# Optimization experiments

Measured on AMD Instinct MI355X. Metric: run time of the kernel, lower is better.

## Reference

```python
import jax, jax.numpy as jnp
import numpy as np

EMB = 1024
NHEAD = 16
HEAD_DIM = EMB // NHEAD  # 64
L = 2048
NEG = -1e30


def setup_inputs() -> dict:
    key = jax.random.key(0)
    ks = jax.random.split(key, 8)
    # xavier_uniform bound for square [EMB, EMB] matrices
    bound = float(np.sqrt(6.0 / (EMB + EMB)))
    def xavier(k):
        return jax.random.uniform(k, (EMB, EMB), jnp.float32, -bound, bound)
    return {
        "q": jax.random.normal(ks[0], (L, EMB), jnp.float32),
        "k": jax.random.normal(ks[1], (L, EMB), jnp.float32),
        "v": jax.random.normal(ks[2], (L, EMB), jnp.float32),
        "mask": jax.random.randint(ks[3], (NHEAD, L, L), 0, 2) > 0,
        "Wq": xavier(ks[4]),
        "Wk": xavier(ks[5]),
        "Wv": xavier(ks[6]),
        "Wo": xavier(ks[7]),
    }


def reference(q, k, v, mask, Wq, Wk, Wv, Wo):
    scaling = HEAD_DIM ** -0.5
    # F.linear(x, W) = x @ W.T ; reshape to [H, L, D]
    Q = (q @ Wq.T).reshape(L, NHEAD, HEAD_DIM).swapaxes(0, 1)
    K = (k @ Wk.T).reshape(L, NHEAD, HEAD_DIM).swapaxes(0, 1)
    V = (v @ Wv.T).reshape(L, NHEAD, HEAD_DIM).swapaxes(0, 1)
    scores = jnp.einsum("hld,hmd->hlm", Q, K) * scaling  # [H, L, L]
    scores = jnp.where(mask, jnp.asarray(NEG, scores.dtype), scores)
    p = jax.nn.softmax(scores, axis=-1)
    # attn_mask=True: multiplicative re-mask after softmax (custom path)
    p = p * (~mask).astype(p.dtype)
    # dropout is a no-op in eval mode
    attn_out = jnp.einsum("hlm,hmd->hld", p, V)  # [H, L, D]
    attn_out = attn_out.swapaxes(0, 1).reshape(L, EMB)
    return attn_out @ Wo.T
```

## Files before the change

kernel.cpp:

```cpp
#include <hip/hip_runtime.h>
#include <stdint.h>

#define EMB   1024
#define NHEAD 16
#define HDIM  64
#define SEQ   2048

typedef unsigned short ushort_t;
typedef unsigned int   uint32;
typedef unsigned long long ull_t;
typedef __attribute__((ext_vector_type(8))) short bfrag;
typedef __attribute__((ext_vector_type(4))) float ffrag;

#define MFMA(a, b, c) __builtin_amdgcn_mfma_f32_16x16x32_bf16((a), (b), (c), 0, 0, 0)

__device__ inline ushort_t f2bf(float f) {
  uint32 u = __float_as_uint(f);
  u += 0x7FFFu + ((u >> 16) & 1u);
  return (ushort_t)(u >> 16);
}
__device__ inline uint32 pack2(float a, float b) {
  return (uint32)f2bf(a) | ((uint32)f2bf(b) << 16);
}

__device__ inline void glds16(const ushort_t* g, ushort_t* l) {
  __builtin_amdgcn_global_load_lds(
      (const __attribute__((address_space(1))) uint32*)(uintptr_t)g,
      (__attribute__((address_space(3))) uint32*)(uintptr_t)l, 16, 0, 0);
}

__global__ void detect_mask_kernel(const uint32* __restrict__ mw, int* __restrict__ flag) {
  uint32 w = mw[threadIdx.x];
  bool is4 = (w == 0u) || (w == 1u) || (w == 0x3F800000u);
  unsigned long long bad = __ballot(!is4);
  if (threadIdx.x == 0) flag[0] = (bad == 0ull) ? 1 : 0;
}

__global__ __launch_bounds__(256) void cvt_all(
    const float4* __restrict__ q,  const float4* __restrict__ k,  const float4* __restrict__ v,
    const float4* __restrict__ wq, const float4* __restrict__ wk, const float4* __restrict__ wv,
    const float4* __restrict__ wo,
    uint2* __restrict__ qb,  uint2* __restrict__ kb,  uint2* __restrict__ vb,
    uint2* __restrict__ wqb, uint2* __restrict__ wkb, uint2* __restrict__ wvb,
    uint2* __restrict__ wob)
{
  int t = blockIdx.x * 256 + threadIdx.x;
  int s = blockIdx.y;
  const float4* src; uint2* dst; int n4;
  switch (s) {
    case 0: src = q;  dst = qb;  n4 = (SEQ * EMB) / 4; break;
    case 1: src = k;  dst = kb;  n4 = (SEQ * EMB) / 4; break;
    case 2: src = v;  dst = vb;  n4 = (SEQ * EMB) / 4; break;
    case 3: src = wq; dst = wqb; n4 = (EMB * EMB) / 4; break;
    case 4: src = wk; dst = wkb; n4 = (EMB * EMB) / 4; break;
    case 5: src = wv; dst = wvb; n4 = (EMB * EMB) / 4; break;
    default: src = wo; dst = wob; n4 = (EMB * EMB) / 4; break;
  }
  if (t >= n4) return;
  float4 f = src[t];
  uint2 o; o.x = pack2(f.x, f.y); o.y = pack2(f.z, f.w);
  dst[t] = o;
}

template<int MODE>
__global__ __launch_bounds__(256) void gemm128(
    const ushort_t* __restrict__ A, const ushort_t* __restrict__ B,
    void* __restrict__ Cp)
{
  __shared__ ushort_t As[128 * 64];
  __shared__ ushort_t Bs[128 * 64];

  const int tid = threadIdx.x, lane = tid & 63, w = tid >> 6;
  const int m0 = blockIdx.y * 128, n0 = blockIdx.x * 128;
  const int wm = (w >> 1) * 64, wn = (w & 1) * 64;
  const int col = lane & 15, g = lane >> 4, kg8 = g * 8;

  int srow[4], scol[4], sdst[4];
  #pragma unroll
  for (int it = 0; it < 4; ++it) {
    int p = w * 256 + it * 64 + lane;
    int row = p >> 3, pc = p & 7;
    srow[it] = row;
    scol[it] = (pc ^ (row & 7)) * 8;
    sdst[it] = p * 8;
  }

  ffrag acc[4][4] = {};

  for (int k0 = 0; k0 < EMB; k0 += 64) {
    __syncthreads();
    #pragma unroll
    for (int it = 0; it < 4; ++it) {
      glds16(A + (size_t)(m0 + srow[it]) * EMB + k0 + scol[it], &As[sdst[it]]);
      glds16(B + (size_t)(n0 + srow[it]) * EMB + k0 + scol[it], &Bs[sdst[it]]);
    }
    __syncthreads();

    #pragma unroll
    for (int c = 0; c < 2; ++c) {
      bfrag av[4], bv[4];
      #pragma unroll
      for (int t = 0; t < 4; ++t) {
        int ra = wm + t * 16 + col;
        av[t] = *(const bfrag*)&As[ra * 64 + ((c * 4 + g) ^ (ra & 7)) * 8];
        int rb = wn + t * 16 + col;
        bv[t] = *(const bfrag*)&Bs[rb * 64 + ((c * 4 + g) ^ (rb & 7)) * 8];
      }
      #pragma unroll
      for (int tm = 0; tm < 4; ++tm)
        #pragma unroll
        for (int tn = 0; tn < 4; ++tn)
          acc[tm][tn] = MFMA(av[tm], bv[tn], acc[tm][tn]);
    }
  }

  const int rbase = g * 4;
  #pragma unroll
  for (int tm = 0; tm < 4; ++tm)
    #pragma unroll
    for (int tn = 0; tn < 4; ++tn)
      #pragma unroll
      for (int r = 0; r < 4; ++r) {
        int m = m0 + wm + tm * 16 + rbase + r;
        int n = n0 + wn + tn * 16 + col;
        float vv = acc[tm][tn][r];
        if (MODE == 0) {
          ((ushort_t*)Cp)[((size_t)(n >> 6) * SEQ + m) * HDIM + (n & 63)] = f2bf(vv);
        } else if (MODE == 1) {
          ((ushort_t*)Cp)[((size_t)(m >> 6) * HDIM + (m & 63)) * SEQ + n] = f2bf(vv);
        } else {
          ((float*)Cp)[(size_t)m * EMB + n] = vv;
        }
      }
}

__global__ __launch_bounds__(256) void attn_mfma(
    const ushort_t* __restrict__ Qb,
    const ushort_t* __restrict__ Kb,
    const ushort_t* __restrict__ Vtb,
    const void* __restrict__ maskp,
    const int* __restrict__ flagp,
    ushort_t* __restrict__ attnb)
{
  __shared__ ushort_t Qs[64][72];
  __shared__ ushort_t Ks[64][72];
  __shared__ ushort_t Vs[64][72];
  __shared__ ushort_t Ps[4][16 * 72];
  __shared__ ushort_t Msk[64][4];

  const int tid  = threadIdx.x;
  const int lane = tid & 63;
  const int w    = tid >> 6;
  const int h    = blockIdx.y;
  const int l0   = blockIdx.x * 64;
  const int use32 = *flagp;
  const int srow = tid >> 2, sseg = (tid & 3) * 16;
  const int col  = lane & 15, g = lane >> 4, kg8 = g * 8, rbase = g * 4;

  const uint32* mask32 = (const uint32*)maskp;
  const unsigned char* mask8 = (const unsigned char*)maskp;

  {
    const uint4* pq = (const uint4*)(Qb + ((size_t)h * SEQ + l0 + srow) * HDIM + sseg);
    uint4 q0 = pq[0], q1 = pq[1];
    *(uint4*)&Qs[srow][sseg] = q0; *(uint4*)&Qs[srow][sseg + 8] = q1;
  }
  __syncthreads();

  bfrag qf[2];
  qf[0] = *(const bfrag*)&Qs[w * 16 + col][kg8];
  qf[1] = *(const bfrag*)&Qs[w * 16 + col][32 + kg8];

  float mrow[4], lrow[4];
  ffrag oacc[4] = {};
  #pragma unroll
  for (int r = 0; r < 4; ++r) { mrow[r] = -1e30f; lrow[r] = 0.f; }

  ushort_t* pq_ = &Ps[w][0];

  for (int kt = 0; kt < SEQ; kt += 64) {
    const uint4* pk = (const uint4*)(Kb + ((size_t)h * SEQ + kt + srow) * HDIM + sseg);
    uint4 k0v = pk[0], k1v = pk[1];
    const uint4* pv = (const uint4*)(Vtb + ((size_t)h * HDIM + srow) * SEQ + kt + sseg);
    uint4 v0v = pv[0], v1v = pv[1];

    ushort_t mv = 0;
    if (use32) {
      const uint4* mp = (const uint4*)(mask32 + ((size_t)h * SEQ + l0 + srow) * SEQ + kt + sseg);
      uint4 a0 = mp[0], a1 = mp[1], a2 = mp[2], a3 = mp[3];
      uint32 aw[16] = {a0.x,a0.y,a0.z,a0.w, a1.x,a1.y,a1.z,a1.w,
                       a2.x,a2.y,a2.z,a2.w, a3.x,a3.y,a3.z,a3.w};
      #pragma unroll
      for (int i = 0; i < 16; ++i) mv |= (ushort_t)((aw[i] != 0u) ? 1u : 0u) << i;
    } else {
      const uint4* bp = (const uint4*)(mask8 + ((size_t)h * SEQ + l0 + srow) * SEQ + kt + sseg);
      uint4 b0 = bp[0];
      uint32 bw[4] = {b0.x, b0.y, b0.z, b0.w};
      #pragma unroll
      for (int i = 0; i < 16; ++i)
        mv |= (ushort_t)((((bw[i >> 2] >> ((i & 3) * 8)) & 0xFFu) != 0u) ? 1u : 0u) << i;
    }

    __syncthreads();
    *(uint4*)&Ks[srow][sseg] = k0v; *(uint4*)&Ks[srow][sseg + 8] = k1v;
    *(uint4*)&Vs[srow][sseg] = v0v; *(uint4*)&Vs[srow][sseg + 8] = v1v;
    Msk[srow][tid & 3] = mv;
    __syncthreads();

    ffrag s[4] = {};
    #pragma unroll
    for (int c = 0; c < 2; ++c)
      #pragma unroll
      for (int tn = 0; tn < 4; ++tn) {
        bfrag kf = *(const bfrag*)&Ks[tn * 16 + col][c * 32 + kg8];
        s[tn] = MFMA(qf[c], kf, s[tn]);
      }

    float sv[4][4];
    float rmax[4] = {-1e30f, -1e30f, -1e30f, -1e30f};
    #pragma unroll
    for (int r = 0; r < 4; ++r) {
      ull_t ms = *(const ull_t*)&Msk[w * 16 + rbase + r][0];
      #pragma unroll
      for (int tn = 0; tn < 4; ++tn) {
        ushort_t m16 = (ushort_t)(ms >> (16 * tn));
        bool msk = ((m16 >> col) & 1) != 0;
        float x = s[tn][r] * 0.125f;
        x = msk ? -1e30f : x;
        sv[tn][r] = x;
        rmax[r] = fmaxf(rmax[r], x);
      }
    }
    #pragma unroll
    for (int r = 0; r < 4; ++r)
      #pragma unroll
      for (int off = 1; off < 16; off <<= 1)
        rmax[r] = fmaxf(rmax[r], __shfl_xor(rmax[r], off, 64));

    float alpha[4], rsum[4] = {0.f, 0.f, 0.f, 0.f};
    #pragma unroll
    for (int r = 0; r < 4; ++r) {
      float mnew = fmaxf(mrow[r], rmax[r]);
      alpha[r] = __expf(mrow[r] - mnew);
      mrow[r] = mnew;
    }

    #pragma unroll
    for (int tn = 0; tn < 4; ++tn)
      #pragma unroll
      for (int r = 0; r < 4; ++r) {
        float p = __expf(sv[tn][r] - mrow[r]);
        rsum[r] += p;
        pq_[(rbase + r) * 72 + tn * 16 + col] = f2bf(p);
      }
    #pragma unroll
    for (int r = 0; r < 4; ++r) {
      #pragma unroll
      for (int off = 1; off < 16; off <<= 1)
        rsum[r] += __shfl_xor(rsum[r], off, 64);
      lrow[r] = lrow[r] * alpha[r] + rsum[r];
    }
    #pragma unroll
    for (int tn = 0; tn < 4; ++tn)
      #pragma unroll
      for (int r = 0; r < 4; ++r)
        oacc[tn][r] *= alpha[r];

    #pragma unroll
    for (int c = 0; c < 2; ++c) {
      bfrag af = *(const bfrag*)&pq_[col * 72 + c * 32 + kg8];
      #pragma unroll
      for (int tn = 0; tn < 4; ++tn) {
        bfrag vf = *(const bfrag*)&Vs[tn * 16 + col][c * 32 + kg8];
        oacc[tn] = MFMA(af, vf, oacc[tn]);
      }
    }
  }

  float inv[4];
  #pragma unroll
  for (int r = 0; r < 4; ++r)
    inv[r] = (mrow[r] > -1e30f) ? (1.0f / lrow[r]) : 0.0f;
  #pragma unroll
  for (int tn = 0; tn < 4; ++tn)
    #pragma unroll
    for (int r = 0; r < 4; ++r) {
      int qg = l0 + w * 16 + rbase + r;
      attnb[(size_t)qg * EMB + h * HDIM + tn * 16 + col] = f2bf(oacc[tn][r] * inv[r]);
    }
}

extern "C" void kernel_launch(void* const* d_in, const int* in_sizes, int n_in,
                              void* d_out, int out_size, void* d_ws, size_t ws_size,
                              hipStream_t stream) {
  const float* q    = (const float*)d_in[0];
  const float* k    = (const float*)d_in[1];
  const float* v    = (const float*)d_in[2];
  const void*  mask =               d_in[3];
  const float* Wq   = (const float*)d_in[4];
  const float* Wk   = (const float*)d_in[5];
  const float* Wv   = (const float*)d_in[6];
  const float* Wo   = (const float*)d_in[7];

  char* ws = (char*)d_ws;
  const size_t MB = 1024 * 1024;
  ushort_t* qb    = (ushort_t*)(ws);
  ushort_t* kb    = (ushort_t*)(ws + 4  * MB);
  ushort_t* vb    = (ushort_t*)(ws + 8  * MB);
  ushort_t* Wqb   = (ushort_t*)(ws + 12 * MB);
  ushort_t* Wkb   = (ushort_t*)(ws + 14 * MB);
  ushort_t* Wvb   = (ushort_t*)(ws + 16 * MB);
  ushort_t* Wob   = (ushort_t*)(ws + 18 * MB);
  ushort_t* Qb    = (ushort_t*)(ws + 20 * MB);
  ushort_t* Kb    = (ushort_t*)(ws + 24 * MB);
  ushort_t* Vtb   = (ushort_t*)(ws + 28 * MB);
  ushort_t* attnb = qb;
  int*      flag  = (int*)(ws + 32 * MB);

  detect_mask_kernel<<<1, 64, 0, stream>>>((const uint32*)mask, flag);

  cvt_all<<<dim3((SEQ * EMB / 4 + 255) / 256, 7), 256, 0, stream>>>(
      (const float4*)q, (const float4*)k, (const float4*)v,
      (const float4*)Wq, (const float4*)Wk, (const float4*)Wv, (const float4*)Wo,
      (uint2*)qb, (uint2*)kb, (uint2*)vb,
      (uint2*)Wqb, (uint2*)Wkb, (uint2*)Wvb, (uint2*)Wob);

  gemm128<0><<<dim3(EMB / 128, SEQ / 128), 256, 0, stream>>>(qb, Wqb, (void*)Qb);
  gemm128<0><<<dim3(EMB / 128, SEQ / 128), 256, 0, stream>>>(kb, Wkb, (void*)Kb);
  gemm128<1><<<dim3(SEQ / 128, EMB / 128), 256, 0, stream>>>(Wvb, vb, (void*)Vtb);

  attn_mfma<<<dim3(SEQ / 64, NHEAD), 256, 0, stream>>>(Qb, Kb, Vtb, mask, flag, attnb);

  gemm128<2><<<dim3(EMB / 128, SEQ / 128), 256, 0, stream>>>(attnb, Wob, d_out);
}
```

Before: 519.1 us.

## Double-buffer K/V via async LDS loads, prefetch mask, merge QKV GEMM launches

The attention kernel now stages K and V tiles into double-buffered, XOR-swizzled shared memory with global_load_lds, prefetching the next tile while computing the current one. This cuts the loop to one barrier per iteration. Mask words are prefetched one iteration ahead into registers and spread across lanes with shuffles, which replaces the shared Msk array. The Q tile now goes through the per-wave P buffer, and the three QKV projection GEMMs are merged into a single launch. Together these aim to hide global load latency and reduce barrier and launch overhead, at the cost of more registers and a wasted prefetch on the last iteration.

```diff
diff --git a/kernel.cpp b/kernel.cpp
--- a/kernel.cpp
+++ b/kernel.cpp
@@ -8,7 +8,6 @@
 
 typedef unsigned short ushort_t;
 typedef unsigned int   uint32;
-typedef unsigned long long ull_t;
 typedef __attribute__((ext_vector_type(8))) short bfrag;
 typedef __attribute__((ext_vector_type(4))) float ffrag;
 
@@ -63,17 +62,11 @@
 }
 
 template<int MODE>
-__global__ __launch_bounds__(256) void gemm128(
-    const ushort_t* __restrict__ A, const ushort_t* __restrict__ B,
-    void* __restrict__ Cp)
-{
-  __shared__ ushort_t As[128 * 64];
-  __shared__ ushort_t Bs[128 * 64];
-
+__device__ inline void gemm_body(const ushort_t* A, const ushort_t* B, void* Cp,
+                                 int m0, int n0, ushort_t* As, ushort_t* Bs) {
   const int tid = threadIdx.x, lane = tid & 63, w = tid >> 6;
-  const int m0 = blockIdx.y * 128, n0 = blockIdx.x * 128;
   const int wm = (w >> 1) * 64, wn = (w & 1) * 64;
-  const int col = lane & 15, g = lane >> 4, kg8 = g * 8;
+  const int col = lane & 15, g = lane >> 4;
 
   int srow[4], scol[4], sdst[4];
   #pragma unroll
@@ -134,6 +127,31 @@
       }
 }
 
+__global__ __launch_bounds__(256) void gemm_qkv(
+    const ushort_t* __restrict__ qb, const ushort_t* __restrict__ kb, const ushort_t* __restrict__ vb,
+    const ushort_t* __restrict__ Wqb, const ushort_t* __restrict__ Wkb, const ushort_t* __restrict__ Wvb,
+    ushort_t* __restrict__ Qb, ushort_t* __restrict__ Kb, ushort_t* __restrict__ Vtb)
+{
+  __shared__ ushort_t As[128 * 64];
+  __shared__ ushort_t Bs[128 * 64];
+  const int z = blockIdx.y, bid = blockIdx.x;
+  if (z == 0) {
+    gemm_body<0>(qb, Wqb, Qb, (bid >> 3) * 128, (bid & 7) * 128, As, Bs);
+  } else if (z == 1) {
+    gemm_body<0>(kb, Wkb, Kb, (bid >> 3) * 128, (bid & 7) * 128, As, Bs);
+  } else {
+    gemm_body<1>(Wvb, vb, Vtb, (bid & 7) * 128, (bid >> 3) * 128, As, Bs);
+  }
+}
+
+__global__ __launch_bounds__(256) void gemm_out(
+    const ushort_t* __restrict__ A, const ushort_t* __restrict__ B, float* __restrict__ C)
+{
+  __shared__ ushort_t As[128 * 64];
+  __shared__ ushort_t Bs[128 * 64];
+  gemm_body<2>(A, B, (void*)C, blockIdx.y * 128, blockIdx.x * 128, As, Bs);
+}
+
 __global__ __launch_bounds__(256) void attn_mfma(
     const ushort_t* __restrict__ Qb,
     const ushort_t* __restrict__ Kb,
@@ -142,11 +160,8 @@
     const int* __restrict__ flagp,
     ushort_t* __restrict__ attnb)
 {
-  __shared__ ushort_t Qs[64][72];
-  __shared__ ushort_t Ks[64][72];
-  __shared__ ushort_t Vs[64][72];
+  __shared__ ushort_t KVs[2][2][64 * 64];
   __shared__ ushort_t Ps[4][16 * 72];
-  __shared__ ushort_t Msk[64][4];
 
   const int tid  = threadIdx.x;
   const int lane = tid & 63;
@@ -154,65 +169,88 @@
   const int h    = blockIdx.y;
   const int l0   = blockIdx.x * 64;
   const int use32 = *flagp;
-  const int srow = tid >> 2, sseg = (tid & 3) * 16;
   const int col  = lane & 15, g = lane >> 4, kg8 = g * 8, rbase = g * 4;
 
   const uint32* mask32 = (const uint32*)maskp;
   const unsigned char* mask8 = (const unsigned char*)maskp;
 
+  ushort_t* pw = &Ps[w][0];
+
   {
-    const uint4* pq = (const uint4*)(Qb + ((size_t)h * SEQ + l0 + srow) * HDIM + sseg);
+    int rl = lane >> 2, seg = (lane & 3) * 16;
+    const uint4* pq = (const uint4*)(Qb + ((size_t)h * SEQ + l0 + w * 16 + rl) * HDIM + seg);
     uint4 q0 = pq[0], q1 = pq[1];
-    *(uint4*)&Qs[srow][sseg] = q0; *(uint4*)&Qs[srow][sseg + 8] = q1;
-  }
-  __syncthreads();
-
+    *(uint4*)&pw[rl * 72 + seg] = q0;
+    *(uint4*)&pw[rl * 72 + seg + 8] = q1;
+  }
   bfrag qf[2];
-  qf[0] = *(const bfrag*)&Qs[w * 16 + col][kg8];
-  qf[1] = *(const bfrag*)&Qs[w * 16 + col][32 + kg8];
+  qf[0] = *(const bfrag*)&pw[col * 72 + kg8];
+  qf[1] = *(const bfrag*)&pw[col * 72 + 32 + kg8];
+
+  auto stage_kv = [&](int kt_, int buf) {
+    #pragma unroll
+    for (int it = 0; it < 2; ++it) {
+      int p = it * 256 + tid;
+      int row = p >> 3, pc = p & 7;
+      int sc = (pc ^ (row & 7)) * 8;
+      glds16(Kb + ((size_t)h * SEQ + kt_ + row) * HDIM + sc, &KVs[buf][0][p * 8]);
+      glds16(Vtb + ((size_t)h * HDIM + row) * SEQ + kt_ + sc, &KVs[buf][1][p * 8]);
+    }
+  };
+  stage_kv(0, 0);
+
+  const int mrl = lane >> 2, mseg = (lane & 3) * 16;
+  const size_t mrow_off = ((size_t)h * SEQ + l0 + w * 16 + mrl) * SEQ + mseg;
+  uint4 ma0, ma1, ma2, ma3;
+  if (use32) {
+    const uint4* mp = (const uint4*)(mask32 + mrow_off);
+    ma0 = mp[0]; ma1 = mp[1]; ma2 = mp[2]; ma3 = mp[3];
+  } else {
+    ma0 = *(const uint4*)(mask8 + mrow_off);
+  }
 
   float mrow[4], lrow[4];
   ffrag oacc[4] = {};
   #pragma unroll
   for (int r = 0; r < 4; ++r) { mrow[r] = -1e30f; lrow[r] = 0.f; }
 
-  ushort_t* pq_ = &Ps[w][0];
-
-  for (int kt = 0; kt < SEQ; kt += 64) {
-    const uint4* pk = (const uint4*)(Kb + ((size_t)h * SEQ + kt + srow) * HDIM + sseg);
-    uint4 k0v = pk[0], k1v = pk[1];
-    const uint4* pv = (const uint4*)(Vtb + ((size_t)h * HDIM + srow) * SEQ + kt + sseg);
-    uint4 v0v = pv[0], v1v = pv[1];
+  for (int t = 0; t < 32; ++t) {
+    const int buf = t & 1;
+    __syncthreads();
+    stage_kv(((t + 1) & 31) * 64, buf ^ 1);
+
+    const ushort_t* Kc = &KVs[buf][0][0];
+    const ushort_t* Vc = &KVs[buf][1][0];
 
     ushort_t mv = 0;
     if (use32) {
-      const uint4* mp = (const uint4*)(mask32 + ((size_t)h * SEQ + l0 + srow) * SEQ + kt + sseg);
-      uint4 a0 = mp[0], a1 = mp[1], a2 = mp[2], a3 = mp[3];
-      uint32 aw[16] = {a0.x,a0.y,a0.z,a0.w, a1.x,a1.y,a1.z,a1.w,
-                       a2.x,a2.y,a2.z,a2.w, a3.x,a3.y,a3.z,a3.w};
+      uint32 aw[16] = {ma0.x,ma0.y,ma0.z,ma0.w, ma1.x,ma1.y,ma1.z,ma1.w,
+                       ma2.x,ma2.y,ma2.z,ma2.w, ma3.x,ma3.y,ma3.z,ma3.w};
       #pragma unroll
       for (int i = 0; i < 16; ++i) mv |= (ushort_t)((aw[i] != 0u) ? 1u : 0u) << i;
     } else {
-      const uint4* bp = (const uint4*)(mask8 + ((size_t)h * SEQ + l0 + srow) * SEQ + kt + sseg);
-      uint4 b0 = bp[0];
-      uint32 bw[4] = {b0.x, b0.y, b0.z, b0.w};
+      uint32 bw[4] = {ma0.x, ma0.y, ma0.z, ma0.w};
       #pragma unroll
       for (int i = 0; i < 16; ++i)
         mv |= (ushort_t)((((bw[i >> 2] >> ((i & 3) * 8)) & 0xFFu) != 0u) ? 1u : 0u) << i;
     }
-
-    __syncthreads();
-    *(uint4*)&Ks[srow][sseg] = k0v; *(uint4*)&Ks[srow][sseg + 8] = k1v;
-    *(uint4*)&Vs[srow][sseg] = v0v; *(uint4*)&Vs[srow][sseg + 8] = v1v;
-    Msk[srow][tid & 3] = mv;
-    __syncthreads();
+    {
+      const int ktn = ((t + 1) & 31) * 64;
+      if (use32) {
+        const uint4* mp = (const uint4*)(mask32 + mrow_off + ktn);
+        ma0 = mp[0]; ma1 = mp[1]; ma2 = mp[2]; ma3 = mp[3];
+      } else {
+        ma0 = *(const uint4*)(mask8 + mrow_off + ktn);
+      }
+    }
 
     ffrag s[4] = {};
     #pragma unroll
     for (int c = 0; c < 2; ++c)
       #pragma unroll
       for (int tn = 0; tn < 4; ++tn) {
-        bfrag kf = *(const bfrag*)&Ks[tn * 16 + col][c * 32 + kg8];
+        int row = tn * 16 + col;
+        bfrag kf = *(const bfrag*)&Kc[row * 64 + ((c * 4 + g) ^ (row & 7)) * 8];
         s[tn] = MFMA(qf[c], kf, s[tn]);
       }
 
@@ -220,10 +258,9 @@
     float rmax[4] = {-1e30f, -1e30f, -1e30f, -1e30f};
     #pragma unroll
     for (int r = 0; r < 4; ++r) {
-      ull_t ms = *(const ull_t*)&Msk[w * 16 + rbase + r][0];
       #pragma unroll
       for (int tn = 0; tn < 4; ++tn) {
-        ushort_t m16 = (ushort_t)(ms >> (16 * tn));
+        int m16 = __shfl((int)mv, (rbase + r) * 4 + tn, 64);
         bool msk = ((m16 >> col) & 1) != 0;
         float x = s[tn][r] * 0.125f;
         x = msk ? -1e30f : x;
@@ -251,7 +288,7 @@
       for (int r = 0; r < 4; ++r) {
         float p = __expf(sv[tn][r] - mrow[r]);
         rsum[r] += p;
-        pq_[(rbase + r) * 72 + tn * 16 + col] = f2bf(p);
+        pw[(rbase + r) * 72 + tn * 16 + col] = f2bf(p);
       }
     #pragma unroll
     for (int r = 0; r < 4; ++r) {
@@ -268,10 +305,11 @@
 
     #pragma unroll
     for (int c = 0; c < 2; ++c) {
-      bfrag af = *(const bfrag*)&pq_[col * 72 + c * 32 + kg8];
+      bfrag af = *(const bfrag*)&pw[col * 72 + c * 32 + kg8];
       #pragma unroll
       for (int tn = 0; tn < 4; ++tn) {
-        bfrag vf = *(const bfrag*)&Vs[tn * 16 + col][c * 32 + kg8];
+        int row = tn * 16 + col;
+        bfrag vf = *(const bfrag*)&Vc[row * 64 + ((c * 4 + g) ^ (row & 7)) * 8];
         oacc[tn] = MFMA(af, vf, oacc[tn]);
       }
     }
@@ -325,11 +363,9 @@
       (uint2*)qb, (uint2*)kb, (uint2*)vb,
       (uint2*)Wqb, (uint2*)Wkb, (uint2*)Wvb, (uint2*)Wob);
 
-  gemm128<0><<<dim3(EMB / 128, SEQ / 128), 256, 0, stream>>>(qb, Wqb, (void*)Qb);
-  gemm128<0><<<dim3(EMB / 128, SEQ / 128), 256, 0, stream>>>(kb, Wkb, (void*)Kb);
-  gemm128<1><<<dim3(SEQ / 128, EMB / 128), 256, 0, stream>>>(Wvb, vb, (void*)Vtb);
+  gemm_qkv<<<dim3(128, 3), 256, 0, stream>>>(qb, kb, vb, Wqb, Wkb, Wvb, Qb, Kb, Vtb);
 
   attn_mfma<<<dim3(SEQ / 64, NHEAD), 256, 0, stream>>>(Qb, Kb, Vtb, mask, flag, attnb);
 
-  gemm128<2><<<dim3(EMB / 128, SEQ / 128), 256, 0, stream>>>(attnb, Wob, d_out);
-}
+  gemm_out<<<dim3(EMB / 128, SEQ / 128), 256, 0, stream>>>(attnb, Wob, (float*)d_out);
+}
```

Measured after the change: 486.3 us. -6.3%, faster.
